# Performance work log

Measured on AMD Instinct MI355X. Metric: run time of the kernel, lower is better.

Reference implementation:

```python
import jax, jax.numpy as jnp
import numpy as np

N_NODES = 50000
N_EDGES = 800000
IN_DIM, HIDDEN, Z_DIM = 32, 64, 32


def gcn_conv(x, W, b, src, dst, n):
    """PyG-style GCNConv: h = D^{-1/2}(A+I)D^{-1/2} (x W) + b."""
    h = x @ W  # [N, out]
    loop = jnp.arange(n, dtype=src.dtype)
    s = jnp.concatenate([src, loop])  # add self-loops
    d = jnp.concatenate([dst, loop])
    deg = jax.ops.segment_sum(jnp.ones(s.shape, h.dtype), d, num_segments=n)
    dinv = jax.lax.rsqrt(jnp.maximum(deg, jnp.asarray(1.0, h.dtype)))
    norm = dinv[s] * dinv[d]                       # [E+N]
    msg = h[s] * norm[:, None]                     # gather + scale
    out = jax.ops.segment_sum(msg, d, num_segments=n)  # scatter-add
    return out + b


def setup_inputs() -> dict:
    key = jax.random.key(0)
    ks = jax.random.split(key, 8)
    sc = lambda fan_in: 1.0 / np.sqrt(fan_in)
    x = jax.random.normal(ks[0], (N_NODES, IN_DIM), jnp.float32)
    edge_index = jax.random.randint(ks[1], (2, N_EDGES), 0, N_NODES, jnp.int64)
    W1 = jax.random.normal(ks[2], (IN_DIM, HIDDEN), jnp.float32) * sc(IN_DIM)
    b1 = jnp.zeros((HIDDEN,), jnp.float32)
    W2 = jax.random.normal(ks[3], (HIDDEN, HIDDEN), jnp.float32) * sc(HIDDEN)
    b2 = jnp.zeros((HIDDEN,), jnp.float32)
    W_mu = jax.random.normal(ks[4], (HIDDEN, Z_DIM), jnp.float32) * sc(HIDDEN)
    b_mu = jnp.zeros((Z_DIM,), jnp.float32)
    W_lv = jax.random.normal(ks[5], (HIDDEN, Z_DIM), jnp.float32) * sc(HIDDEN)
    b_lv = jnp.zeros((Z_DIM,), jnp.float32)
    eps = jax.random.normal(ks[6], (N_NODES, Z_DIM), jnp.float32)
    return {"x": x, "edge_index": edge_index, "W1": W1, "b1": b1, "W2": W2,
            "b2": b2, "W_mu": W_mu, "b_mu": b_mu, "W_lv": W_lv, "b_lv": b_lv,
            "eps": eps}


def reference(x, edge_index, W1, b1, W2, b2, W_mu, b_mu, W_lv, b_lv, eps):
    src, dst = edge_index[0], edge_index[1]
    n = x.shape[0]
    h = jax.nn.relu(gcn_conv(x, W1, b1, src, dst, n))
    h = jax.nn.relu(gcn_conv(h, W2, b2, src, dst, n))
    # dropout p=0.0 -> identity
    mu = gcn_conv(h, W_mu, b_mu, src, dst, n)
    logvar = gcn_conv(h, W_lv, b_lv, src, dst, n)
    z = mu + jnp.exp(0.5 * logvar) * eps  # reparametrize
    return (z, mu, logvar)
```

## Files before the change

### kernel.cpp

```cpp
#include <hip/hip_runtime.h>
#include <math.h>

#define N_NODES 50000
#define N_EDGES 800000
#define IN_DIM 32
#define HIDDEN 64
#define Z_DIM 32
#define SCAN_B 256
#define NB_SCAN ((N_NODES + SCAN_B - 1) / SCAN_B)
#define N_XCD 8
#define NPX ((N_NODES + N_XCD - 1) / N_XCD)
#define SLICE 2048
#define N_SLICE ((N_EDGES + SLICE - 1) / SLICE)
#define SCAT_B (N_SLICE * N_XCD)
#define FB 2048
#define CPAD 16

__device__ __forceinline__ float bf2f(unsigned short u) {
    return __uint_as_float(((unsigned int)u) << 16);
}
__device__ __forceinline__ unsigned short f2bf(float f) {
    unsigned int u = __float_as_uint(f);
    u += 0x7fffu + ((u >> 16) & 1u);
    return (unsigned short)(u >> 16);
}

__device__ __forceinline__ int detect64(const int* raw) {
    int lane = threadIdx.x & 63;
    int odd = raw[2 * lane + 1];
    unsigned long long b = __ballot(odd != 0);
    return (b == 0ULL) ? 1 : 0;
}

__global__ void prep_a_kernel(const float* __restrict__ x, unsigned short* __restrict__ xb,
                              const void* __restrict__ raw, int2* __restrict__ ep0,
                              int* __restrict__ dstc) {
    int is64 = detect64((const int*)raw);
    int i = blockIdx.x * 256 + threadIdx.x;
    if (i < N_NODES * IN_DIM) xb[i] = f2bf(x[i]);
    if (i < N_EDGES) {
        int s, d;
        if (is64) {
            s = (int)((const long long*)raw)[i];
            d = (int)((const long long*)raw)[N_EDGES + i];
        } else {
            s = ((const int*)raw)[i];
            d = ((const int*)raw)[N_EDGES + i];
        }
        ep0[i] = make_int2(s, d);
        dstc[i] = d;
    }
}

__global__ __launch_bounds__(256) void hist_kernel(const int* __restrict__ dstc,
                                                   int* __restrict__ cnt,
                                                   unsigned short* __restrict__ rank) {
    int xcd = blockIdx.x % N_XCD;
    int sl  = blockIdx.x / N_XCD;
    int lo  = xcd * NPX, hi = lo + NPX;
    int base = sl * SLICE;
#pragma unroll
    for (int j = 0; j < SLICE / 256; j++) {
        int e = base + j * 256 + threadIdx.x;
        if (e < N_EDGES) {
            int d = dstc[e];
            if (d >= lo && d < hi)
                rank[e] = (unsigned short)atomicAdd(&cnt[(size_t)d * CPAD], 1);
        }
    }
}

__global__ void scan1_kernel(const int* __restrict__ cnt, int* __restrict__ pre,
                             int* __restrict__ bsum, float* __restrict__ dinv) {
    __shared__ int s[SCAN_B];
    int t = threadIdx.x;
    int g = blockIdx.x * SCAN_B + t;
    int v = (g < N_NODES) ? cnt[(size_t)g * CPAD] : 0;
    if (g < N_NODES) dinv[g] = rsqrtf((float)(v + 1));
    s[t] = v;
    __syncthreads();
    for (int o = 1; o < SCAN_B; o <<= 1) {
        int add = (t >= o) ? s[t - o] : 0;
        __syncthreads();
        s[t] += add;
        __syncthreads();
    }
    if (g < N_NODES) pre[g] = s[t] - v;
    if (t == SCAN_B - 1) bsum[blockIdx.x] = s[t];
}

__global__ void scan23_kernel(int* __restrict__ rowptr, const int* __restrict__ bsum) {
    __shared__ int s[256];
    int t = threadIdx.x;
    int v = (t < NB_SCAN) ? bsum[t] : 0;
    s[t] = v;
    __syncthreads();
    for (int o = 1; o < 256; o <<= 1) {
        int add = (t >= o) ? s[t - o] : 0;
        __syncthreads();
        s[t] += add;
        __syncthreads();
    }
    int excl = s[blockIdx.x] - bsum[blockIdx.x];
    int g = blockIdx.x * SCAN_B + t;
    if (g < N_NODES) rowptr[g] += excl;
    if (g == 0) rowptr[N_NODES] = N_EDGES;
}

__global__ __launch_bounds__(256) void scatter_kernel(
        const int2* __restrict__ ep0, const unsigned short* __restrict__ rank,
        const int* __restrict__ rowptr, const float* __restrict__ dinv,
        int2* __restrict__ ep) {
    int base = blockIdx.x * SLICE;
#pragma unroll
    for (int j = 0; j < SLICE / 256; j++) {
        int e = base + j * 256 + threadIdx.x;
        if (e < N_EDGES) {
            int2 sd = ep0[e];
            int p = rowptr[sd.y] + (int)rank[e];
            ep[p] = make_int2(sd.x, __float_as_int(dinv[sd.x]));
        }
    }
}

__device__ __forceinline__ void agg_body64(int e0, int e1, int2 pr,
                                           const int2* __restrict__ ep,
                                           const uint2* __restrict__ g2,
                                           int lane, float acc[4]) {
    int gsel = lane >> 4;
    int c    = lane & 15;
    for (int base = e0; base < e1; base += 64) {
        int cnt = e1 - base; cnt = cnt > 64 ? 64 : cnt;
        for (int j = 0; j < cnt; j += 16) {
            uint2 fv[4]; float wv[4];
#pragma unroll
            for (int u = 0; u < 4; u++) {
                int idx = j + u * 4 + gsel;
                int cl  = idx < cnt ? idx : cnt - 1;
                int s   = __builtin_amdgcn_ds_bpermute(cl << 2, pr.x);
                int w   = __builtin_amdgcn_ds_bpermute(cl << 2, pr.y);
                wv[u]   = idx < cnt ? __int_as_float(w) : 0.0f;
                fv[u]   = g2[(size_t)s * 16 + c];
            }
#pragma unroll
            for (int u = 0; u < 4; u++) {
                acc[0] = fmaf(wv[u], __uint_as_float(fv[u].x << 16),         acc[0]);
                acc[1] = fmaf(wv[u], __uint_as_float(fv[u].x & 0xffff0000u), acc[1]);
                acc[2] = fmaf(wv[u], __uint_as_float(fv[u].y << 16),         acc[2]);
                acc[3] = fmaf(wv[u], __uint_as_float(fv[u].y & 0xffff0000u), acc[3]);
            }
        }
        int nb = base + 64;
        if (nb + lane < e1) pr = ep[nb + lane];
    }
}

__device__ __forceinline__ void agg_body32(int e0, int e1, int2 pr,
                                           const int2* __restrict__ ep,
                                           const uint2* __restrict__ x2,
                                           int lane, float acc[4]) {
    int gsel = lane >> 3;
    int c    = lane & 7;
    for (int base = e0; base < e1; base += 64) {
        int cnt = e1 - base; cnt = cnt > 64 ? 64 : cnt;
        for (int j = 0; j < cnt; j += 16) {
            uint2 fv[2]; float wv[2];
#pragma unroll
            for (int u = 0; u < 2; u++) {
                int idx = j + u * 8 + gsel;
                int cl  = idx < cnt ? idx : cnt - 1;
                int s   = __builtin_amdgcn_ds_bpermute(cl << 2, pr.x);
                int w   = __builtin_amdgcn_ds_bpermute(cl << 2, pr.y);
                wv[u]   = idx < cnt ? __int_as_float(w) : 0.0f;
                fv[u]   = x2[(size_t)s * 8 + c];
            }
#pragma unroll
            for (int u = 0; u < 2; u++) {
                acc[0] = fmaf(wv[u], __uint_as_float(fv[u].x << 16),         acc[0]);
                acc[1] = fmaf(wv[u], __uint_as_float(fv[u].x & 0xffff0000u), acc[1]);
                acc[2] = fmaf(wv[u], __uint_as_float(fv[u].y << 16),         acc[2]);
                acc[3] = fmaf(wv[u], __uint_as_float(fv[u].y & 0xffff0000u), acc[3]);
            }
        }
        int nb = base + 64;
        if (nb + lane < e1) pr = ep[nb + lane];
    }
}

__global__ __launch_bounds__(256, 4) void fused_layer32_kernel(
        const int* __restrict__ rowptr, const int2* __restrict__ ep,
        const float* __restrict__ dinv, const unsigned short* __restrict__ xb,
        const float* __restrict__ W1, const float* __restrict__ b1,
        unsigned short* __restrict__ out) {
    __shared__ float sq[4 * 32];
    int lane = threadIdx.x & 63;
    int wav  = threadIdx.x >> 6;
    int gsel = lane >> 3;
    int c    = lane & 7;
    const uint2* x2 = (const uint2*)xb;
    float wcol[IN_DIM];
#pragma unroll
    for (int k = 0; k < IN_DIM; k++) wcol[k] = W1[k * 64 + lane];
    float bb = b1[lane];
    int wid = __builtin_amdgcn_readfirstlane((int)((blockIdx.x * blockDim.x + threadIdx.x) >> 6));
    int nw  = (gridDim.x * blockDim.x) >> 6;
    int v = wid;
    if (v >= N_NODES) return;
    int e0 = rowptr[v], e1 = rowptr[v + 1];
    float dv = dinv[v];
    uint2 hv = x2[(size_t)v * 8 + c];
    int2 pr = make_int2(0, 0);
    if (lane < e1 - e0) pr = ep[e0 + lane];
    while (v < N_NODES) {
        int vn = v + nw;
        int e0n = 0, e1n = 0;
        float dvn = 0.0f;
        uint2 hvn = make_uint2(0, 0);
        int2 prn = make_int2(0, 0);
        if (vn < N_NODES) {
            e0n = rowptr[vn]; e1n = rowptr[vn + 1];
            dvn = dinv[vn];
            hvn = x2[(size_t)vn * 8 + c];
            if (lane < e1n - e0n) prn = ep[e0n + lane];
        }
        float sv = (gsel == 0) ? dv : 0.0f;
        float acc[4];
        acc[0] = sv * __uint_as_float(hv.x << 16);
        acc[1] = sv * __uint_as_float(hv.x & 0xffff0000u);
        acc[2] = sv * __uint_as_float(hv.y << 16);
        acc[3] = sv * __uint_as_float(hv.y & 0xffff0000u);
        agg_body32(e0, e1, pr, ep, x2, lane, acc);
#pragma unroll
        for (int i = 0; i < 4; i++) {
            acc[i] += __shfl_xor(acc[i], 8);
            acc[i] += __shfl_xor(acc[i], 16);
            acc[i] += __shfl_xor(acc[i], 32);
        }
        if (lane < 8)
            ((float4*)(sq + wav * 32))[c] =
                make_float4(dv * acc[0], dv * acc[1], dv * acc[2], dv * acc[3]);
        float o = bb;
        const float4* q4 = (const float4*)(sq + wav * 32);
#pragma unroll
        for (int k = 0; k < IN_DIM / 4; k++) {
            float4 t = q4[k];
            o = fmaf(t.x, wcol[4 * k + 0], o);
            o = fmaf(t.y, wcol[4 * k + 1], o);
            o = fmaf(t.z, wcol[4 * k + 2], o);
            o = fmaf(t.w, wcol[4 * k + 3], o);
        }
        out[(size_t)v * 64 + lane] = f2bf(fmaxf(o, 0.0f));
        v = vn; e0 = e0n; e1 = e1n; dv = dvn; hv = hvn; pr = prn;
    }
}

__global__ __launch_bounds__(256, 4) void fused_layer64_kernel(
        const int* __restrict__ rowptr, const int2* __restrict__ ep,
        const float* __restrict__ dinv, const unsigned short* __restrict__ g,
        const float* __restrict__ W, const float* __restrict__ bias,
        unsigned short* __restrict__ out) {
    __shared__ float sq[4 * 64];
    int lane = threadIdx.x & 63;
    int wav  = threadIdx.x >> 6;
    int gsel = lane >> 4;
    int c    = lane & 15;
    const uint2* g2 = (const uint2*)g;
    float wcol[HIDDEN];
#pragma unroll
    for (int k = 0; k < HIDDEN; k++) wcol[k] = W[k * 64 + lane];
    float bb = bias[lane];
    int wid = __builtin_amdgcn_readfirstlane((int)((blockIdx.x * blockDim.x + threadIdx.x) >> 6));
    int nw  = (gridDim.x * blockDim.x) >> 6;
    int v = wid;
    if (v >= N_NODES) return;
    int e0 = rowptr[v], e1 = rowptr[v + 1];
    float dv = dinv[v];
    uint2 hv = g2[(size_t)v * 16 + c];
    int2 pr = make_int2(0, 0);
    if (lane < e1 - e0) pr = ep[e0 + lane];
    while (v < N_NODES) {
        int vn = v + nw;
        int e0n = 0, e1n = 0;
        float dvn = 0.0f;
        uint2 hvn = make_uint2(0, 0);
        int2 prn = make_int2(0, 0);
        if (vn < N_NODES) {
            e0n = rowptr[vn]; e1n = rowptr[vn + 1];
            dvn = dinv[vn];
            hvn = g2[(size_t)vn * 16 + c];
            if (lane < e1n - e0n) prn = ep[e0n + lane];
        }
        float sv = (gsel == 0) ? dv : 0.0f;
        float acc[4];
        acc[0] = sv * __uint_as_float(hv.x << 16);
        acc[1] = sv * __uint_as_float(hv.x & 0xffff0000u);
        acc[2] = sv * __uint_as_float(hv.y << 16);
        acc[3] = sv * __uint_as_float(hv.y & 0xffff0000u);
        agg_body64(e0, e1, pr, ep, g2, lane, acc);
#pragma unroll
        for (int i = 0; i < 4; i++) {
            acc[i] += __shfl_xor(acc[i], 16);
            acc[i] += __shfl_xor(acc[i], 32);
        }
        if (lane < 16)
            ((float4*)(sq + wav * 64))[c] =
                make_float4(dv * acc[0], dv * acc[1], dv * acc[2], dv * acc[3]);
        float o = bb;
        const float4* q4 = (const float4*)(sq + wav * 64);
#pragma unroll
        for (int k = 0; k < HIDDEN / 4; k++) {
            float4 t = q4[k];
            o = fmaf(t.x, wcol[4 * k + 0], o);
            o = fmaf(t.y, wcol[4 * k + 1], o);
            o = fmaf(t.z, wcol[4 * k + 2], o);
            o = fmaf(t.w, wcol[4 * k + 3], o);
        }
        out[(size_t)v * 64 + lane] = f2bf(fmaxf(o, 0.0f));
        v = vn; e0 = e0n; e1 = e1n; dv = dvn; hv = hvn; pr = prn;
    }
}

__global__ __launch_bounds__(256, 4) void fused_head_kernel(
        const int* __restrict__ rowptr, const int2* __restrict__ ep,
        const float* __restrict__ dinv, const unsigned short* __restrict__ g,
        const float* __restrict__ Wmu, const float* __restrict__ Wlv,
        const float* __restrict__ bmu, const float* __restrict__ blv,
        const float* __restrict__ eps, float* __restrict__ outz) {
    __shared__ float sq[4 * 64];
    int lane = threadIdx.x & 63;
    int wav  = threadIdx.x >> 6;
    int gsel = lane >> 4;
    int c    = lane & 15;
    int f = lane & 31;
    bool hi = lane >= 32;
    const uint2* g2 = (const uint2*)g;
    float wcol[HIDDEN];
#pragma unroll
    for (int k = 0; k < HIDDEN; k++)
        wcol[k] = hi ? Wlv[k * 32 + f] : Wmu[k * 32 + f];
    float bb = hi ? blv[f] : bmu[f];
    float* z  = outz;
    float* mu = outz + (size_t)N_NODES * Z_DIM;
    float* lv = outz + 2 * (size_t)N_NODES * Z_DIM;
    int wid = __builtin_amdgcn_readfirstlane((int)((blockIdx.x * blockDim.x + threadIdx.x) >> 6));
    int nw  = (gridDim.x * blockDim.x) >> 6;
    int v = wid;
    if (v >= N_NODES) return;
    int e0 = rowptr[v], e1 = rowptr[v + 1];
    float dv = dinv[v];
    uint2 hv = g2[(size_t)v * 16 + c];
    int2 pr = make_int2(0, 0);
    if (lane < e1 - e0) pr = ep[e0 + lane];
    while (v < N_NODES) {
        int vn = v + nw;
        int e0n = 0, e1n = 0;
        float dvn = 0.0f;
        uint2 hvn = make_uint2(0, 0);
        int2 prn = make_int2(0, 0);
        if (vn < N_NODES) {
            e0n = rowptr[vn]; e1n = rowptr[vn + 1];
            dvn = dinv[vn];
            hvn = g2[(size_t)vn * 16 + c];
            if (lane < e1n - e0n) prn = ep[e0n + lane];
        }
        float sv = (gsel == 0) ? dv : 0.0f;
        float acc[4];
        acc[0] = sv * __uint_as_float(hv.x << 16);
        acc[1] = sv * __uint_as_float(hv.x & 0xffff0000u);
        acc[2] = sv * __uint_as_float(hv.y << 16);
        acc[3] = sv * __uint_as_float(hv.y & 0xffff0000u);
        agg_body64(e0, e1, pr, ep, g2, lane, acc);
#pragma unroll
        for (int i = 0; i < 4; i++) {
            acc[i] += __shfl_xor(acc[i], 16);
            acc[i] += __shfl_xor(acc[i], 32);
        }
        if (lane < 16)
            ((float4*)(sq + wav * 64))[c] =
                make_float4(dv * acc[0], dv * acc[1], dv * acc[2], dv * acc[3]);
        float m = bb;
        const float4* q4 = (const float4*)(sq + wav * 64);
#pragma unroll
        for (int k = 0; k < HIDDEN / 4; k++) {
            float4 t = q4[k];
            m = fmaf(t.x, wcol[4 * k + 0], m);
            m = fmaf(t.y, wcol[4 * k + 1], m);
            m = fmaf(t.z, wcol[4 * k + 2], m);
            m = fmaf(t.w, wcol[4 * k + 3], m);
        }
        float ev = eps[(size_t)v * Z_DIM + f];
        float t  = expf(0.5f * m) * ev;
        float tlo = __shfl(t, lane | 32);
        size_t o = (size_t)v * Z_DIM + f;
        if (!hi) { mu[o] = m; z[o] = m + tlo; }
        else     { lv[o] = m; }
        v = vn; e0 = e0n; e1 = e1n; dv = dvn; hv = hvn; pr = prn;
    }
}

extern "C" void kernel_launch(void* const* d_in, const int* in_sizes, int n_in,
                              void* d_out, int out_size, void* d_ws, size_t ws_size,
                              hipStream_t stream) {
    const float* x   = (const float*)d_in[0];
    const void*  ei  = d_in[1];
    const float* W1  = (const float*)d_in[2];
    const float* b1  = (const float*)d_in[3];
    const float* W2  = (const float*)d_in[4];
    const float* b2  = (const float*)d_in[5];
    const float* Wmu = (const float*)d_in[6];
    const float* bmu = (const float*)d_in[7];
    const float* Wlv = (const float*)d_in[8];
    const float* blv = (const float*)d_in[9];
    const float* eps = (const float*)d_in[10];
    float* out = (float*)d_out;
    (void)in_sizes; (void)n_in; (void)out_size; (void)ws_size;

    char* ws = (char*)d_ws;
    size_t off = 0;
    auto alloc = [&](size_t bytes) -> void* {
        void* p = ws + off;
        off += (bytes + 255) & ~(size_t)255;
        return p;
    };
    int2*           ep     = (int2*)alloc(sizeof(int2) * N_EDGES);
    int2*           ep0    = (int2*)alloc(sizeof(int2) * N_EDGES);
    int*            dstc   = (int*)alloc(sizeof(int) * N_EDGES);
    unsigned short* rank   = (unsigned short*)alloc(sizeof(short) * N_EDGES);
    int*            rowptr = (int*)alloc(sizeof(int) * (N_NODES + 1));
    int*            cnt    = (int*)alloc(sizeof(int) * (size_t)N_NODES * CPAD);
    float*          dinv   = (float*)alloc(sizeof(float) * N_NODES);
    int*            bsum   = (int*)alloc(sizeof(int) * 256);
    unsigned short* xb     = (unsigned short*)alloc(sizeof(short) * (size_t)N_NODES * IN_DIM);
    unsigned short* G      = (unsigned short*)alloc(sizeof(short) * (size_t)N_NODES * HIDDEN);
    unsigned short* H      = (unsigned short*)alloc(sizeof(short) * (size_t)N_NODES * HIDDEN);

    hipMemsetAsync(cnt, 0, sizeof(int) * (size_t)N_NODES * CPAD, stream);
    prep_a_kernel<<<(N_NODES * IN_DIM + 255) / 256, 256, 0, stream>>>(x, xb, ei, ep0, dstc);
    hist_kernel<<<SCAT_B, 256, 0, stream>>>(dstc, cnt, rank);
    scan1_kernel<<<NB_SCAN, SCAN_B, 0, stream>>>(cnt, rowptr, bsum, dinv);
    scan23_kernel<<<NB_SCAN, SCAN_B, 0, stream>>>(rowptr, bsum);
    scatter_kernel<<<N_SLICE, 256, 0, stream>>>(ep0, rank, rowptr, dinv, ep);
    fused_layer32_kernel<<<FB, 256, 0, stream>>>(rowptr, ep, dinv, xb, W1, b1, H);
    fused_layer64_kernel<<<FB, 256, 0, stream>>>(rowptr, ep, dinv, H, W2, b2, G);
    fused_head_kernel<<<FB, 256, 0, stream>>>(rowptr, ep, dinv, G, Wmu, Wlv, bmu, blv, eps, out);
}
```

Baseline: 234.1 us.

## Fold memset and block-sum scan into kernels, pack edges to ushort, widen gathers

Zeroing of the count array moves into the prep kernel, replacing the separate memset. The block-sum scan kernel is removed; each consumer kernel redoes the small bsum scan in shared memory and adds the block offset itself. The edge pairs are stored as ushort2, which shrinks intermediate traffic and relies on node ids fitting in 16 bits. The aggregation loops gather 16-byte uint4 rows with edges staged through LDS instead of ds_bpermute, so each lane holds 8 accumulators and needs one more shuffle-reduction step. The trade-off is redundant scan work in every block, extra LDS use and more register pressure.

```diff
diff --git a/kernel.cpp b/kernel.cpp
--- a/kernel.cpp
+++ b/kernel.cpp
@@ -16,9 +16,6 @@
 #define FB 2048
 #define CPAD 16
 
-__device__ __forceinline__ float bf2f(unsigned short u) {
-    return __uint_as_float(((unsigned int)u) << 16);
-}
 __device__ __forceinline__ unsigned short f2bf(float f) {
     unsigned int u = __float_as_uint(f);
     u += 0x7fffu + ((u >> 16) & 1u);
@@ -32,12 +29,34 @@
     return (b == 0ULL) ? 1 : 0;
 }
 
+__device__ __forceinline__ void fma8(float w, uint4 f, float acc[8]) {
+    acc[0] = fmaf(w, __uint_as_float(f.x << 16),         acc[0]);
+    acc[1] = fmaf(w, __uint_as_float(f.x & 0xffff0000u), acc[1]);
+    acc[2] = fmaf(w, __uint_as_float(f.y << 16),         acc[2]);
+    acc[3] = fmaf(w, __uint_as_float(f.y & 0xffff0000u), acc[3]);
+    acc[4] = fmaf(w, __uint_as_float(f.z << 16),         acc[4]);
+    acc[5] = fmaf(w, __uint_as_float(f.z & 0xffff0000u), acc[5]);
+    acc[6] = fmaf(w, __uint_as_float(f.w << 16),         acc[6]);
+    acc[7] = fmaf(w, __uint_as_float(f.w & 0xffff0000u), acc[7]);
+}
+__device__ __forceinline__ void mul8(float w, uint4 f, float acc[8]) {
+    acc[0] = w * __uint_as_float(f.x << 16);
+    acc[1] = w * __uint_as_float(f.x & 0xffff0000u);
+    acc[2] = w * __uint_as_float(f.y << 16);
+    acc[3] = w * __uint_as_float(f.y & 0xffff0000u);
+    acc[4] = w * __uint_as_float(f.z << 16);
+    acc[5] = w * __uint_as_float(f.z & 0xffff0000u);
+    acc[6] = w * __uint_as_float(f.w << 16);
+    acc[7] = w * __uint_as_float(f.w & 0xffff0000u);
+}
+
 __global__ void prep_a_kernel(const float* __restrict__ x, unsigned short* __restrict__ xb,
-                              const void* __restrict__ raw, int2* __restrict__ ep0,
-                              int* __restrict__ dstc) {
+                              const void* __restrict__ raw, ushort2* __restrict__ ep0,
+                              int* __restrict__ cnt) {
     int is64 = detect64((const int*)raw);
     int i = blockIdx.x * 256 + threadIdx.x;
     if (i < N_NODES * IN_DIM) xb[i] = f2bf(x[i]);
+    if (i < N_NODES * CPAD) cnt[i] = 0;
     if (i < N_EDGES) {
         int s, d;
         if (is64) {
@@ -47,12 +66,11 @@
             s = ((const int*)raw)[i];
             d = ((const int*)raw)[N_EDGES + i];
         }
-        ep0[i] = make_int2(s, d);
-        dstc[i] = d;
-    }
-}
-
-__global__ __launch_bounds__(256) void hist_kernel(const int* __restrict__ dstc,
+        ep0[i] = make_ushort2((unsigned short)s, (unsigned short)d);
+    }
+}
+
+__global__ __launch_bounds__(256) void hist_kernel(const ushort2* __restrict__ ep0,
                                                    int* __restrict__ cnt,
                                                    unsigned short* __restrict__ rank) {
     int xcd = blockIdx.x % N_XCD;
@@ -63,7 +81,7 @@
     for (int j = 0; j < SLICE / 256; j++) {
         int e = base + j * 256 + threadIdx.x;
         if (e < N_EDGES) {
-            int d = dstc[e];
+            int d = ep0[e].y;
             if (d >= lo && d < hi)
                 rank[e] = (unsigned short)atomicAdd(&cnt[(size_t)d * CPAD], 1);
         }
@@ -89,115 +107,108 @@
     if (t == SCAN_B - 1) bsum[blockIdx.x] = s[t];
 }
 
-__global__ void scan23_kernel(int* __restrict__ rowptr, const int* __restrict__ bsum) {
-    __shared__ int s[256];
-    int t = threadIdx.x;
-    int v = (t < NB_SCAN) ? bsum[t] : 0;
-    s[t] = v;
-    __syncthreads();
-    for (int o = 1; o < 256; o <<= 1) {
-        int add = (t >= o) ? s[t - o] : 0;
-        __syncthreads();
-        s[t] += add;
-        __syncthreads();
-    }
-    int excl = s[blockIdx.x] - bsum[blockIdx.x];
-    int g = blockIdx.x * SCAN_B + t;
-    if (g < N_NODES) rowptr[g] += excl;
-    if (g == 0) rowptr[N_NODES] = N_EDGES;
-}
+#define BSUM_SCAN_PROLOGUE(bsum, sb, sx)                                    \
+    {                                                                       \
+        int t_ = threadIdx.x;                                               \
+        int bv_ = (t_ < NB_SCAN) ? bsum[t_] : 0;                            \
+        sb[t_] = bv_;                                                       \
+        __syncthreads();                                                    \
+        for (int o_ = 1; o_ < 256; o_ <<= 1) {                              \
+            int a_ = (t_ >= o_) ? sb[t_ - o_] : 0;                          \
+            __syncthreads();                                                \
+            sb[t_] += a_;                                                   \
+            __syncthreads();                                                \
+        }                                                                   \
+        sx[t_] = sb[t_] - bv_;                                              \
+        __syncthreads();                                                    \
+    }
 
 __global__ __launch_bounds__(256) void scatter_kernel(
-        const int2* __restrict__ ep0, const unsigned short* __restrict__ rank,
-        const int* __restrict__ rowptr, const float* __restrict__ dinv,
-        int2* __restrict__ ep) {
+        const ushort2* __restrict__ ep0, const unsigned short* __restrict__ rank,
+        const int* __restrict__ pre, const int* __restrict__ bsum,
+        const float* __restrict__ dinv, int2* __restrict__ ep) {
+    __shared__ int sb[256];
+    __shared__ int sx[256];
+    BSUM_SCAN_PROLOGUE(bsum, sb, sx)
     int base = blockIdx.x * SLICE;
 #pragma unroll
     for (int j = 0; j < SLICE / 256; j++) {
         int e = base + j * 256 + threadIdx.x;
         if (e < N_EDGES) {
-            int2 sd = ep0[e];
-            int p = rowptr[sd.y] + (int)rank[e];
-            ep[p] = make_int2(sd.x, __float_as_int(dinv[sd.x]));
-        }
-    }
-}
-
-__device__ __forceinline__ void agg_body64(int e0, int e1, int2 pr,
-                                           const int2* __restrict__ ep,
-                                           const uint2* __restrict__ g2,
-                                           int lane, float acc[4]) {
-    int gsel = lane >> 4;
-    int c    = lane & 15;
-    for (int base = e0; base < e1; base += 64) {
-        int cnt = e1 - base; cnt = cnt > 64 ? 64 : cnt;
+            ushort2 sd = ep0[e];
+            int d = sd.y;
+            int p = pre[d] + sx[d >> 8] + (int)rank[e];
+            int s = sd.x;
+            ep[p] = make_int2(s, __float_as_int(dinv[s]));
+        }
+    }
+}
+
+__device__ __forceinline__ void agg64(int e0, int e1, int2 pr,
+                                      const int2* __restrict__ ep,
+                                      const uint4* __restrict__ g4,
+                                      int2* eb, int lane, int gsel, int c,
+                                      float acc[8]) {
+    for (int b0 = e0; b0 < e1; b0 += 64) {
+        int cnt = e1 - b0; cnt = cnt > 64 ? 64 : cnt;
+        eb[lane] = pr;
         for (int j = 0; j < cnt; j += 16) {
-            uint2 fv[4]; float wv[4];
-#pragma unroll
-            for (int u = 0; u < 4; u++) {
-                int idx = j + u * 4 + gsel;
-                int cl  = idx < cnt ? idx : cnt - 1;
-                int s   = __builtin_amdgcn_ds_bpermute(cl << 2, pr.x);
-                int w   = __builtin_amdgcn_ds_bpermute(cl << 2, pr.y);
-                wv[u]   = idx < cnt ? __int_as_float(w) : 0.0f;
-                fv[u]   = g2[(size_t)s * 16 + c];
-            }
-#pragma unroll
-            for (int u = 0; u < 4; u++) {
-                acc[0] = fmaf(wv[u], __uint_as_float(fv[u].x << 16),         acc[0]);
-                acc[1] = fmaf(wv[u], __uint_as_float(fv[u].x & 0xffff0000u), acc[1]);
-                acc[2] = fmaf(wv[u], __uint_as_float(fv[u].y << 16),         acc[2]);
-                acc[3] = fmaf(wv[u], __uint_as_float(fv[u].y & 0xffff0000u), acc[3]);
-            }
-        }
-        int nb = base + 64;
-        if (nb + lane < e1) pr = ep[nb + lane];
-    }
-}
-
-__device__ __forceinline__ void agg_body32(int e0, int e1, int2 pr,
-                                           const int2* __restrict__ ep,
-                                           const uint2* __restrict__ x2,
-                                           int lane, float acc[4]) {
-    int gsel = lane >> 3;
-    int c    = lane & 7;
-    for (int base = e0; base < e1; base += 64) {
-        int cnt = e1 - base; cnt = cnt > 64 ? 64 : cnt;
-        for (int j = 0; j < cnt; j += 16) {
-            uint2 fv[2]; float wv[2];
-#pragma unroll
-            for (int u = 0; u < 2; u++) {
-                int idx = j + u * 8 + gsel;
-                int cl  = idx < cnt ? idx : cnt - 1;
-                int s   = __builtin_amdgcn_ds_bpermute(cl << 2, pr.x);
-                int w   = __builtin_amdgcn_ds_bpermute(cl << 2, pr.y);
-                wv[u]   = idx < cnt ? __int_as_float(w) : 0.0f;
-                fv[u]   = x2[(size_t)s * 8 + c];
-            }
-#pragma unroll
-            for (int u = 0; u < 2; u++) {
-                acc[0] = fmaf(wv[u], __uint_as_float(fv[u].x << 16),         acc[0]);
-                acc[1] = fmaf(wv[u], __uint_as_float(fv[u].x & 0xffff0000u), acc[1]);
-                acc[2] = fmaf(wv[u], __uint_as_float(fv[u].y << 16),         acc[2]);
-                acc[3] = fmaf(wv[u], __uint_as_float(fv[u].y & 0xffff0000u), acc[3]);
-            }
-        }
-        int nb = base + 64;
-        if (nb + lane < e1) pr = ep[nb + lane];
+            int2 ew0 = eb[j + gsel];
+            int2 ew1 = eb[j + 8 + gsel];
+            uint4 f0 = g4[(size_t)ew0.x * 8 + c];
+            uint4 f1 = g4[(size_t)ew1.x * 8 + c];
+            fma8(__int_as_float(ew0.y), f0, acc);
+            fma8(__int_as_float(ew1.y), f1, acc);
+        }
+        if (b0 + 64 < e1) {
+            pr = make_int2(0, 0);
+            int idx = b0 + 64 + lane;
+            if (idx < e1) pr = ep[idx];
+        }
+    }
+}
+
+__device__ __forceinline__ void agg32(int e0, int e1, int2 pr,
+                                      const int2* __restrict__ ep,
+                                      const uint4* __restrict__ x4,
+                                      int2* eb, int lane, int gsel, int c,
+                                      float acc[8]) {
+    for (int b0 = e0; b0 < e1; b0 += 64) {
+        int cnt = e1 - b0; cnt = cnt > 64 ? 64 : cnt;
+        eb[lane] = pr;
+        for (int j = 0; j < cnt; j += 32) {
+            int2 ew0 = eb[j + gsel];
+            int2 ew1 = eb[j + 16 + gsel];
+            uint4 f0 = x4[(size_t)ew0.x * 4 + c];
+            uint4 f1 = x4[(size_t)ew1.x * 4 + c];
+            fma8(__int_as_float(ew0.y), f0, acc);
+            fma8(__int_as_float(ew1.y), f1, acc);
+        }
+        if (b0 + 64 < e1) {
+            pr = make_int2(0, 0);
+            int idx = b0 + 64 + lane;
+            if (idx < e1) pr = ep[idx];
+        }
     }
 }
 
 __global__ __launch_bounds__(256, 4) void fused_layer32_kernel(
-        const int* __restrict__ rowptr, const int2* __restrict__ ep,
-        const float* __restrict__ dinv, const unsigned short* __restrict__ xb,
+        const int* __restrict__ pre, const int* __restrict__ bsum,
+        const int2* __restrict__ ep, const float* __restrict__ dinv,
+        const unsigned short* __restrict__ xb,
         const float* __restrict__ W1, const float* __restrict__ b1,
         unsigned short* __restrict__ out) {
-    __shared__ float sq[4 * 32];
+    __shared__ int sb[256];
+    __shared__ int sx[256];
+    __shared__ int2 ebuf[4][64];
+    __shared__ float sq[4][32];
+    BSUM_SCAN_PROLOGUE(bsum, sb, sx)
     int lane = threadIdx.x & 63;
     int wav  = threadIdx.x >> 6;
-    int gsel = lane >> 3;
-    int c    = lane & 7;
-    const uint2* x2 = (const uint2*)xb;
+    int gsel = lane >> 2;
+    int c    = lane & 3;
+    const uint4* x4 = (const uint4*)xb;
+    int2* eb = &ebuf[wav][0];
     float wcol[IN_DIM];
 #pragma unroll
     for (int k = 0; k < IN_DIM; k++) wcol[k] = W1[k * 64 + lane];
@@ -206,48 +217,50 @@
     int nw  = (gridDim.x * blockDim.x) >> 6;
     int v = wid;
     if (v >= N_NODES) return;
-    int e0 = rowptr[v], e1 = rowptr[v + 1];
+    int e0 = pre[v] + sx[v >> 8];
+    int e1 = (v + 1 < N_NODES) ? pre[v + 1] + sx[(v + 1) >> 8] : N_EDGES;
     float dv = dinv[v];
-    uint2 hv = x2[(size_t)v * 8 + c];
+    uint4 hv = x4[(size_t)v * 4 + c];
     int2 pr = make_int2(0, 0);
     if (lane < e1 - e0) pr = ep[e0 + lane];
     while (v < N_NODES) {
         int vn = v + nw;
         int e0n = 0, e1n = 0;
         float dvn = 0.0f;
-        uint2 hvn = make_uint2(0, 0);
+        uint4 hvn = make_uint4(0, 0, 0, 0);
         int2 prn = make_int2(0, 0);
         if (vn < N_NODES) {
-            e0n = rowptr[vn]; e1n = rowptr[vn + 1];
+            e0n = pre[vn] + sx[vn >> 8];
+            e1n = (vn + 1 < N_NODES) ? pre[vn + 1] + sx[(vn + 1) >> 8] : N_EDGES;
             dvn = dinv[vn];
-            hvn = x2[(size_t)vn * 8 + c];
+            hvn = x4[(size_t)vn * 4 + c];
             if (lane < e1n - e0n) prn = ep[e0n + lane];
         }
         float sv = (gsel == 0) ? dv : 0.0f;
-        float acc[4];
-        acc[0] = sv * __uint_as_float(hv.x << 16);
-        acc[1] = sv * __uint_as_float(hv.x & 0xffff0000u);
-        acc[2] = sv * __uint_as_float(hv.y << 16);
-        acc[3] = sv * __uint_as_float(hv.y & 0xffff0000u);
-        agg_body32(e0, e1, pr, ep, x2, lane, acc);
-#pragma unroll
-        for (int i = 0; i < 4; i++) {
+        float acc[8];
+        mul8(sv, hv, acc);
+        agg32(e0, e1, pr, ep, x4, eb, lane, gsel, c, acc);
+#pragma unroll
+        for (int i = 0; i < 8; i++) {
+            acc[i] += __shfl_xor(acc[i], 4);
             acc[i] += __shfl_xor(acc[i], 8);
             acc[i] += __shfl_xor(acc[i], 16);
             acc[i] += __shfl_xor(acc[i], 32);
         }
-        if (lane < 8)
-            ((float4*)(sq + wav * 32))[c] =
-                make_float4(dv * acc[0], dv * acc[1], dv * acc[2], dv * acc[3]);
+        if (lane < 4) {
+            float4* qd = (float4*)(&sq[wav][lane * 8]);
+            qd[0] = make_float4(dv * acc[0], dv * acc[1], dv * acc[2], dv * acc[3]);
+            qd[1] = make_float4(dv * acc[4], dv * acc[5], dv * acc[6], dv * acc[7]);
+        }
         float o = bb;
-        const float4* q4 = (const float4*)(sq + wav * 32);
+        const float4* q4 = (const float4*)(&sq[wav][0]);
 #pragma unroll
         for (int k = 0; k < IN_DIM / 4; k++) {
-            float4 t = q4[k];
-            o = fmaf(t.x, wcol[4 * k + 0], o);
-            o = fmaf(t.y, wcol[4 * k + 1], o);
-            o = fmaf(t.z, wcol[4 * k + 2], o);
-            o = fmaf(t.w, wcol[4 * k + 3], o);
+            float4 tq = q4[k];
+            o = fmaf(tq.x, wcol[4 * k + 0], o);
+            o = fmaf(tq.y, wcol[4 * k + 1], o);
+            o = fmaf(tq.z, wcol[4 * k + 2], o);
+            o = fmaf(tq.w, wcol[4 * k + 3], o);
         }
         out[(size_t)v * 64 + lane] = f2bf(fmaxf(o, 0.0f));
         v = vn; e0 = e0n; e1 = e1n; dv = dvn; hv = hvn; pr = prn;
@@ -255,16 +268,22 @@
 }
 
 __global__ __launch_bounds__(256, 4) void fused_layer64_kernel(
-        const int* __restrict__ rowptr, const int2* __restrict__ ep,
-        const float* __restrict__ dinv, const unsigned short* __restrict__ g,
+        const int* __restrict__ pre, const int* __restrict__ bsum,
+        const int2* __restrict__ ep, const float* __restrict__ dinv,
+        const unsigned short* __restrict__ g,
         const float* __restrict__ W, const float* __restrict__ bias,
         unsigned short* __restrict__ out) {
-    __shared__ float sq[4 * 64];
+    __shared__ int sb[256];
+    __shared__ int sx[256];
+    __shared__ int2 ebuf[4][64];
+    __shared__ float sq[4][64];
+    BSUM_SCAN_PROLOGUE(bsum, sb, sx)
     int lane = threadIdx.x & 63;
     int wav  = threadIdx.x >> 6;
-    int gsel = lane >> 4;
-    int c    = lane & 15;
-    const uint2* g2 = (const uint2*)g;
+    int gsel = lane >> 3;
+    int c    = lane & 7;
+    const uint4* g4 = (const uint4*)g;
+    int2* eb = &ebuf[wav][0];
     float wcol[HIDDEN];
 #pragma unroll
     for (int k = 0; k < HIDDEN; k++) wcol[k] = W[k * 64 + lane];
@@ -273,47 +292,49 @@
     int nw  = (gridDim.x * blockDim.x) >> 6;
     int v = wid;
     if (v >= N_NODES) return;
-    int e0 = rowptr[v], e1 = rowptr[v + 1];
+    int e0 = pre[v] + sx[v >> 8];
+    int e1 = (v + 1 < N_NODES) ? pre[v + 1] + sx[(v + 1) >> 8] : N_EDGES;
     float dv = dinv[v];
-    uint2 hv = g2[(size_t)v * 16 + c];
+    uint4 hv = g4[(size_t)v * 8 + c];
     int2 pr = make_int2(0, 0);
     if (lane < e1 - e0) pr = ep[e0 + lane];
     while (v < N_NODES) {
         int vn = v + nw;
         int e0n = 0, e1n = 0;
         float dvn = 0.0f;
-        uint2 hvn = make_uint2(0, 0);
+        uint4 hvn = make_uint4(0, 0, 0, 0);
         int2 prn = make_int2(0, 0);
         if (vn < N_NODES) {
-            e0n = rowptr[vn]; e1n = rowptr[vn + 1];
+            e0n = pre[vn] + sx[vn >> 8];
+            e1n = (vn + 1 < N_NODES) ? pre[vn + 1] + sx[(vn + 1) >> 8] : N_EDGES;
             dvn = dinv[vn];
-            hvn = g2[(size_t)vn * 16 + c];
+            hvn = g4[(size_t)vn * 8 + c];
             if (lane < e1n - e0n) prn = ep[e0n + lane];
         }
         float sv = (gsel == 0) ? dv : 0.0f;
-        float acc[4];
-        acc[0] = sv * __uint_as_float(hv.x << 16);
-        acc[1] = sv * __uint_as_float(hv.x & 0xffff0000u);
-        acc[2] = sv * __uint_as_float(hv.y << 16);
-        acc[3] = sv * __uint_as_float(hv.y & 0xffff0000u);
-        agg_body64(e0, e1, pr, ep, g2, lane, acc);
-#pragma unroll
-        for (int i = 0; i < 4; i++) {
+        float acc[8];
+        mul8(sv, hv, acc);
+        agg64(e0, e1, pr, ep, g4, eb, lane, gsel, c, acc);
+#pragma unroll
+        for (int i = 0; i < 8; i++) {
+            acc[i] += __shfl_xor(acc[i], 8);
             acc[i] += __shfl_xor(acc[i], 16);
             acc[i] += __shfl_xor(acc[i], 32);
         }
-        if (lane < 16)
-            ((float4*)(sq + wav * 64))[c] =
-                make_float4(dv * acc[0], dv * acc[1], dv * acc[2], dv * acc[3]);
+        if (lane < 8) {
+            float4* qd = (float4*)(&sq[wav][lane * 8]);
+            qd[0] = make_float4(dv * acc[0], dv * acc[1], dv * acc[2], dv * acc[3]);
+            qd[1] = make_float4(dv * acc[4], dv * acc[5], dv * acc[6], dv * acc[7]);
+        }
         float o = bb;
-        const float4* q4 = (const float4*)(sq + wav * 64);
+        const float4* q4 = (const float4*)(&sq[wav][0]);
 #pragma unroll
         for (int k = 0; k < HIDDEN / 4; k++) {
-            float4 t = q4[k];
-            o = fmaf(t.x, wcol[4 * k + 0], o);
-            o = fmaf(t.y, wcol[4 * k + 1], o);
-            o = fmaf(t.z, wcol[4 * k + 2], o);
-            o = fmaf(t.w, wcol[4 * k + 3], o);
+            float4 tq = q4[k];
+            o = fmaf(tq.x, wcol[4 * k + 0], o);
+            o = fmaf(tq.y, wcol[4 * k + 1], o);
+            o = fmaf(tq.z, wcol[4 * k + 2], o);
+            o = fmaf(tq.w, wcol[4 * k + 3], o);
         }
         out[(size_t)v * 64 + lane] = f2bf(fmaxf(o, 0.0f));
         v = vn; e0 = e0n; e1 = e1n; dv = dvn; hv = hvn; pr = prn;
@@ -321,19 +342,25 @@
 }
 
 __global__ __launch_bounds__(256, 4) void fused_head_kernel(
-        const int* __restrict__ rowptr, const int2* __restrict__ ep,
-        const float* __restrict__ dinv, const unsigned short* __restrict__ g,
+        const int* __restrict__ pre, const int* __restrict__ bsum,
+        const int2* __restrict__ ep, const float* __restrict__ dinv,
+        const unsigned short* __restrict__ g,
         const float* __restrict__ Wmu, const float* __restrict__ Wlv,
         const float* __restrict__ bmu, const float* __restrict__ blv,
         const float* __restrict__ eps, float* __restrict__ outz) {
-    __shared__ float sq[4 * 64];
+    __shared__ int sb[256];
+    __shared__ int sx[256];
+    __shared__ int2 ebuf[4][64];
+    __shared__ float sq[4][64];
+    BSUM_SCAN_PROLOGUE(bsum, sb, sx)
     int lane = threadIdx.x & 63;
     int wav  = threadIdx.x >> 6;
-    int gsel = lane >> 4;
-    int c    = lane & 15;
+    int gsel = lane >> 3;
+    int c    = lane & 7;
     int f = lane & 31;
     bool hi = lane >= 32;
-    const uint2* g2 = (const uint2*)g;
+    const uint4* g4 = (const uint4*)g;
+    int2* eb = &ebuf[wav][0];
     float wcol[HIDDEN];
 #pragma unroll
     for (int k = 0; k < HIDDEN; k++)
@@ -346,47 +373,49 @@
     int nw  = (gridDim.x * blockDim.x) >> 6;
     int v = wid;
     if (v >= N_NODES) return;
-    int e0 = rowptr[v], e1 = rowptr[v + 1];
+    int e0 = pre[v] + sx[v >> 8];
+    int e1 = (v + 1 < N_NODES) ? pre[v + 1] + sx[(v + 1) >> 8] : N_EDGES;
     float dv = dinv[v];
-    uint2 hv = g2[(size_t)v * 16 + c];
+    uint4 hv = g4[(size_t)v * 8 + c];
     int2 pr = make_int2(0, 0);
     if (lane < e1 - e0) pr = ep[e0 + lane];
     while (v < N_NODES) {
         int vn = v + nw;
         int e0n = 0, e1n = 0;
         float dvn = 0.0f;
-        uint2 hvn = make_uint2(0, 0);
+        uint4 hvn = make_uint4(0, 0, 0, 0);
         int2 prn = make_int2(0, 0);
         if (vn < N_NODES) {
-            e0n = rowptr[vn]; e1n = rowptr[vn + 1];
+            e0n = pre[vn] + sx[vn >> 8];
+            e1n = (vn + 1 < N_NODES) ? pre[vn + 1] + sx[(vn + 1) >> 8] : N_EDGES;
             dvn = dinv[vn];
-            hvn = g2[(size_t)vn * 16 + c];
+            hvn = g4[(size_t)vn * 8 + c];
             if (lane < e1n - e0n) prn = ep[e0n + lane];
         }
         float sv = (gsel == 0) ? dv : 0.0f;
-        float acc[4];
-        acc[0] = sv * __uint_as_float(hv.x << 16);
-        acc[1] = sv * __uint_as_float(hv.x & 0xffff0000u);
-        acc[2] = sv * __uint_as_float(hv.y << 16);
-        acc[3] = sv * __uint_as_float(hv.y & 0xffff0000u);
-        agg_body64(e0, e1, pr, ep, g2, lane, acc);
-#pragma unroll
-        for (int i = 0; i < 4; i++) {
+        float acc[8];
+        mul8(sv, hv, acc);
+        agg64(e0, e1, pr, ep, g4, eb, lane, gsel, c, acc);
+#pragma unroll
+        for (int i = 0; i < 8; i++) {
+            acc[i] += __shfl_xor(acc[i], 8);
             acc[i] += __shfl_xor(acc[i], 16);
             acc[i] += __shfl_xor(acc[i], 32);
         }
-        if (lane < 16)
-            ((float4*)(sq + wav * 64))[c] =
-                make_float4(dv * acc[0], dv * acc[1], dv * acc[2], dv * acc[3]);
+        if (lane < 8) {
+            float4* qd = (float4*)(&sq[wav][lane * 8]);
+            qd[0] = make_float4(dv * acc[0], dv * acc[1], dv * acc[2], dv * acc[3]);
+            qd[1] = make_float4(dv * acc[4], dv * acc[5], dv * acc[6], dv * acc[7]);
+        }
         float m = bb;
-        const float4* q4 = (const float4*)(sq + wav * 64);
+        const float4* q4 = (const float4*)(&sq[wav][0]);
 #pragma unroll
         for (int k = 0; k < HIDDEN / 4; k++) {
-            float4 t = q4[k];
-            m = fmaf(t.x, wcol[4 * k + 0], m);
-            m = fmaf(t.y, wcol[4 * k + 1], m);
-            m = fmaf(t.z, wcol[4 * k + 2], m);
-            m = fmaf(t.w, wcol[4 * k + 3], m);
+            float4 tq = q4[k];
+            m = fmaf(tq.x, wcol[4 * k + 0], m);
+            m = fmaf(tq.y, wcol[4 * k + 1], m);
+            m = fmaf(tq.z, wcol[4 * k + 2], m);
+            m = fmaf(tq.w, wcol[4 * k + 3], m);
         }
         float ev = eps[(size_t)v * Z_DIM + f];
         float t  = expf(0.5f * m) * ev;
@@ -423,10 +452,9 @@
         return p;
     };
     int2*           ep     = (int2*)alloc(sizeof(int2) * N_EDGES);
-    int2*           ep0    = (int2*)alloc(sizeof(int2) * N_EDGES);
-    int*            dstc   = (int*)alloc(sizeof(int) * N_EDGES);
+    ushort2*        ep0    = (ushort2*)alloc(sizeof(ushort2) * N_EDGES);
     unsigned short* rank   = (unsigned short*)alloc(sizeof(short) * N_EDGES);
-    int*            rowptr = (int*)alloc(sizeof(int) * (N_NODES + 1));
+    int*            pre    = (int*)alloc(sizeof(int) * (N_NODES + 1));
     int*            cnt    = (int*)alloc(sizeof(int) * (size_t)N_NODES * CPAD);
     float*          dinv   = (float*)alloc(sizeof(float) * N_NODES);
     int*            bsum   = (int*)alloc(sizeof(int) * 256);
@@ -434,13 +462,11 @@
     unsigned short* G      = (unsigned short*)alloc(sizeof(short) * (size_t)N_NODES * HIDDEN);
     unsigned short* H      = (unsigned short*)alloc(sizeof(short) * (size_t)N_NODES * HIDDEN);
 
-    hipMemsetAsync(cnt, 0, sizeof(int) * (size_t)N_NODES * CPAD, stream);
-    prep_a_kernel<<<(N_NODES * IN_DIM + 255) / 256, 256, 0, stream>>>(x, xb, ei, ep0, dstc);
-    hist_kernel<<<SCAT_B, 256, 0, stream>>>(dstc, cnt, rank);
-    scan1_kernel<<<NB_SCAN, SCAN_B, 0, stream>>>(cnt, rowptr, bsum, dinv);
-    scan23_kernel<<<NB_SCAN, SCAN_B, 0, stream>>>(rowptr, bsum);
-    scatter_kernel<<<N_SLICE, 256, 0, stream>>>(ep0, rank, rowptr, dinv, ep);
-    fused_layer32_kernel<<<FB, 256, 0, stream>>>(rowptr, ep, dinv, xb, W1, b1, H);
-    fused_layer64_kernel<<<FB, 256, 0, stream>>>(rowptr, ep, dinv, H, W2, b2, G);
-    fused_head_kernel<<<FB, 256, 0, stream>>>(rowptr, ep, dinv, G, Wmu, Wlv, bmu, blv, eps, out);
-}
+    prep_a_kernel<<<(N_NODES * IN_DIM + 255) / 256, 256, 0, stream>>>(x, xb, ei, ep0, cnt);
+    hist_kernel<<<SCAT_B, 256, 0, stream>>>(ep0, cnt, rank);
+    scan1_kernel<<<NB_SCAN, SCAN_B, 0, stream>>>(cnt, pre, bsum, dinv);
+    scatter_kernel<<<N_SLICE, 256, 0, stream>>>(ep0, rank, pre, bsum, dinv, ep);
+    fused_layer32_kernel<<<FB, 256, 0, stream>>>(pre, bsum, ep, dinv, xb, W1, b1, H);
+    fused_layer64_kernel<<<FB, 256, 0, stream>>>(pre, bsum, ep, dinv, H, W2, b2, G);
+    fused_head_kernel<<<FB, 256, 0, stream>>>(pre, bsum, ep, dinv, G, Wmu, Wlv, bmu, blv, eps, out);
+}
```

Result: slower. 250.9 us (+7.2%).
